# Performance work log

Hardware: AMD Instinct MI355X
Metric: run time of the kernel (lower is better)

## Reference

```python
import jax, jax.numpy as jnp
import numpy as np

Q_LEN, SRC_LEN, B = 512, 2048, 32
Q_SIZE, V_SIZE, OUT_SIZE = 1024, 1024, 1024


def setup_inputs() -> dict:
    key = jax.random.key(0)
    k1, k2, k3, k4, k5, k6 = jax.random.split(key, 6)
    s1 = 1.0 / np.sqrt(Q_SIZE)
    s2 = 1.0 / np.sqrt(Q_SIZE + V_SIZE)
    return {
        "query": jax.random.normal(k1, (Q_LEN, B, Q_SIZE), dtype=jnp.float32),
        "values": jax.random.normal(k2, (SRC_LEN, B, V_SIZE), dtype=jnp.float32),
        "W1": jax.random.uniform(k3, (V_SIZE, Q_SIZE), dtype=jnp.float32, minval=-s1, maxval=s1),
        "b1": jax.random.uniform(k4, (V_SIZE,), dtype=jnp.float32, minval=-s1, maxval=s1),
        "W2": jax.random.uniform(k5, (OUT_SIZE, Q_SIZE + V_SIZE), dtype=jnp.float32, minval=-s2, maxval=s2),
        "b2": jax.random.uniform(k6, (OUT_SIZE,), dtype=jnp.float32, minval=-s2, maxval=s2),
    }


def reference(query, values, W1, b1, W2, b2):
    # query: [q_len, B, Dq]; values: [src_len, B, Dv]
    query_resize = jnp.einsum('qbd,vd->qbv', query, W1) + b1  # [q_len, B, Dv]
    # attn scores: [B, q_len, src_len]
    attn_scores = jnp.einsum('qbv,sbv->bqs', query_resize, values)
    attn = jax.nn.softmax(attn_scores, axis=-1)
    # attended values back to seq-first layout: [q_len, B, Dv]
    attended = jnp.einsum('bqs,sbv->qbv', attn, values)
    query_feed = jnp.concatenate([attended, query], axis=-1)  # [q_len, B, Dv+Dq]
    out = jnp.tanh(jnp.einsum('qbf,of->qbo', query_feed, W2) + b2)
    return out
```

## Files before the change

### kernel.cpp

```cpp
#include <hip/hip_runtime.h>
#include <hip/hip_bf16.h>


typedef __attribute__((ext_vector_type(8))) short bf16x8;
typedef __attribute__((ext_vector_type(4))) float f32x4;

__device__ __forceinline__ ushort f2bf(float x) {
    unsigned u = __builtin_bit_cast(unsigned, x);
    u += 0x7FFFu + ((u >> 16) & 1u);
    return (ushort)(u >> 16);
}
__device__ __forceinline__ float bf2f(ushort h) {
    unsigned u = (unsigned)h << 16;
    return __builtin_bit_cast(float, u);
}
__device__ __forceinline__ void async16(const ushort* g, ushort* l) {
    __builtin_amdgcn_global_load_lds(
        (const __attribute__((address_space(1))) unsigned int*)g,
        (__attribute__((address_space(3))) unsigned int*)l, 16, 0, 0);
}

#define WAITVM(N) asm volatile("s_waitcnt vmcnt(" #N ")" ::: "memory")
#define BAR() do { __builtin_amdgcn_sched_barrier(0); \
                   __builtin_amdgcn_s_barrier();      \
                   __builtin_amdgcn_sched_barrier(0); } while (0)

#define RD_A(QM)                                                              \
  _Pragma("unroll") for (int mi = 0; mi < 4; ++mi)                            \
  _Pragma("unroll") for (int w = 0; w < 2; ++w) {                             \
    const int row_ = (QM)*128 + wmg*64 + mi*16 + lr;                          \
    av[mi][w] = *(const bf16x8*)(bufc + row_*64 + (((w*4+lg)^(lr&7))*8));     \
  }
#define RD_B(QN)                                                              \
  _Pragma("unroll") for (int nj = 0; nj < 2; ++nj)                            \
  _Pragma("unroll") for (int w = 0; w < 2; ++w) {                             \
    const int row_ = (QN)*128 + wnd*32 + nj*16 + lr;                          \
    bv[nj][w] = *(const bf16x8*)(bufc + 16384 + row_*64 + (((w*4+lg)^(lr&7))*8)); \
  }
#define MM(QM,QN)                                                             \
  __builtin_amdgcn_s_setprio(1);                                              \
  _Pragma("unroll") for (int w = 0; w < 2; ++w)                               \
  _Pragma("unroll") for (int mi = 0; mi < 4; ++mi)                            \
  _Pragma("unroll") for (int nj = 0; nj < 2; ++nj)                            \
    acc[(QM)*4+mi][(QN)*2+nj] = __builtin_amdgcn_mfma_f32_16x16x32_bf16(      \
        av[mi][w], bv[nj][w], acc[(QM)*4+mi][(QN)*2+nj], 0, 0, 0);            \
  __builtin_amdgcn_s_setprio(0);

template<int OUTMODE>
__global__ __launch_bounds__(512, 2) void gemm8p(
    const ushort* __restrict__ A0s, const ushort* __restrict__ A1s, const ushort* __restrict__ A2s,
    const ushort* __restrict__ B0s, const ushort* __restrict__ B1s, const ushort* __restrict__ B2s,
    long lda, long ldb, int tps, int nseg,
    const float* __restrict__ bias,
    float* __restrict__ Cf, ushort* __restrict__ Chi, ushort* __restrict__ Clo,
    long ldc, long sAb, long sBb, long sCb)
{
    __shared__ ushort lds[2][32768];

    const int t   = threadIdx.x;
    const int l   = t & 63;
    const int wid = t >> 6;
    const int lr  = l & 15;
    const int lg  = l >> 4;
    const int wmg = wid >> 2;
    const int wnd = wid & 3;

    const int gx = gridDim.x, gy = gridDim.y;
    const int nwg = gx * gy * gridDim.z;
    int w0 = ((int)blockIdx.z * gy + (int)blockIdx.y) * gx + (int)blockIdx.x;
    w0 = (w0 & 7) * (nwg >> 3) + (w0 >> 3);
    const int bx = w0 % gx;
    const int by = (w0 / gx) % gy;
    const int bz = w0 / (gx * gy);

    const long m0 = (long)by * 256;
    const long n0 = (long)bx * 256;

    const ushort* Asg[3] = { A0s + (long)bz * sAb, A1s + (long)bz * sAb, A2s + (long)bz * sAb };
    const ushort* Bsg[3] = { B0s + (long)bz * sBb, B1s + (long)bz * sBb, B2s + (long)bz * sBb };
    const int NTt = nseg * tps;

    const int  rA = t >> 3;
    const long cS = (long)((t & 7) ^ (rA & 7)) * 8;

    auto STAGE = [&](int kt1, bool isB, int half, int destoff) {
        int s2 = (kt1 >= tps) + (kt1 >= 2 * tps);
        long ko = (long)(kt1 - s2 * tps) * 64;
        const ushort* base = isB ? Bsg[s2] : Asg[s2];
        long ld = isB ? ldb : lda;
        long rb = isB ? n0 : m0;
        const ushort* src = base + (rb + half * 128 + rA) * ld + ko + cS;
        ushort* d = &lds[kt1 & 1][destoff + t * 8];
        async16(src, d);
        async16(src + 64 * ld, d + 4096);
    };

    const f32x4 zero = {0.f, 0.f, 0.f, 0.f};
    f32x4 acc[8][4];
#pragma unroll
    for (int i = 0; i < 8; ++i)
#pragma unroll
        for (int j = 0; j < 4; ++j) acc[i][j] = zero;

    STAGE(0, false, 0, 0);
    STAGE(0, true,  0, 16384);
    STAGE(0, true,  1, 24576);
    STAGE(0, false, 1, 8192);

    bf16x8 av[4][2], bv[2][2];

    for (int kt = 0; kt < NTt - 1; ++kt) {
        const ushort* bufc = &lds[kt & 1][0];
        WAITVM(4); BAR();
        STAGE(kt + 1, false, 0, 0);
        RD_A(0); RD_B(0); MM(0, 0);
        WAITVM(4); BAR();
        STAGE(kt + 1, true, 0, 16384);
        RD_B(1); MM(0, 1);
        WAITVM(4); BAR();
        STAGE(kt + 1, true, 1, 24576);
        RD_A(1); MM(1, 1);
        BAR();
        STAGE(kt + 1, false, 1, 8192);
        RD_B(0); MM(1, 0);
    }
    {
        const ushort* bufc = &lds[(NTt - 1) & 1][0];
        WAITVM(4); BAR(); RD_A(0); RD_B(0); MM(0, 0);
        WAITVM(2); BAR(); RD_B(1); MM(0, 1);
        WAITVM(0); BAR(); RD_A(1); MM(1, 1);
        BAR();            RD_B(0); MM(1, 0);
    }

    float*  Cfb = Cf  ? (Cf  + (long)bz * sCb) : nullptr;
    ushort* Chb = Chi ? (Chi + (long)bz * sCb) : nullptr;
    ushort* Clb = Clo ? (Clo + (long)bz * sCb) : nullptr;
#pragma unroll
    for (int qn = 0; qn < 2; ++qn)
#pragma unroll
    for (int nj = 0; nj < 2; ++nj) {
        long n = n0 + qn * 128 + wnd * 32 + nj * 16 + lr;
        float bvs = 0.f;
        if (OUTMODE == 3) bvs = bias[n];
        if (OUTMODE == 2) { if (bias) bvs = bias[n]; }
#pragma unroll
        for (int qm = 0; qm < 2; ++qm)
#pragma unroll
        for (int mi = 0; mi < 4; ++mi) {
            long mb = m0 + qm * 128 + wmg * 64 + mi * 16 + lg * 4;
#pragma unroll
            for (int r = 0; r < 4; ++r) {
                float x = acc[qm * 4 + mi][qn * 2 + nj][r] + bvs;
                long idx = (mb + r) * ldc + n;
                if (OUTMODE == 3) {
                    Cfb[idx] = tanhf(x);
                } else if (OUTMODE == 2) {
                    ushort h = f2bf(x);
                    Chb[idx] = h;
                    if (Clb) Clb[idx] = f2bf(x - bf2f(h));
                } else {
                    Cfb[idx] = x;
                }
            }
        }
    }
}

__global__ __launch_bounds__(256) void split_pair_k(
    const float* __restrict__ in, ushort* __restrict__ hi, ushort* __restrict__ lo, long n4)
{
    long i = (long)blockIdx.x * 256 + threadIdx.x;
    const long stride = (long)gridDim.x * 256;
    for (; i < n4; i += stride) {
        float4 x = ((const float4*)in)[i];
        ushort4 h, lw;
        h.x = f2bf(x.x); lw.x = f2bf(x.x - bf2f(h.x));
        h.y = f2bf(x.y); lw.y = f2bf(x.y - bf2f(h.y));
        h.z = f2bf(x.z); lw.z = f2bf(x.z - bf2f(h.z));
        h.w = f2bf(x.w); lw.w = f2bf(x.w - bf2f(h.w));
        ((ushort4*)hi)[i] = h;
        ((ushort4*)lo)[i] = lw;
    }
}

__global__ __launch_bounds__(256) void values_conv_k(
    const float* __restrict__ values,
    ushort* __restrict__ vhi, ushort* __restrict__ vlo, ushort* __restrict__ vT,
    int b0, int gc)
{
    __shared__ float tile[64][65];
    const int t  = threadIdx.x;
    const int s0 = blockIdx.x * 64;
    const int v0 = blockIdx.y * 64;
    const int bi = blockIdx.z;
    const int b  = b0 + bi;
#pragma unroll
    for (int i = 0; i < 4; ++i) {
        int c = t + i * 256;
        int r = c >> 4;
        int qq = c & 15;
        float4 x = *(const float4*)(values + ((long)(s0 + r) * 32 + b) * 1024 + v0 + qq * 4);
        ushort4 h, lw;
        h.x = f2bf(x.x); lw.x = f2bf(x.x - bf2f(h.x));
        h.y = f2bf(x.y); lw.y = f2bf(x.y - bf2f(h.y));
        h.z = f2bf(x.z); lw.z = f2bf(x.z - bf2f(h.z));
        h.w = f2bf(x.w); lw.w = f2bf(x.w - bf2f(h.w));
        long rowoff = ((long)(s0 + r) * gc + bi) * 1024 + v0 + qq * 4;
        *(ushort4*)(vhi + rowoff) = h;
        *(ushort4*)(vlo + rowoff) = lw;
        tile[r][qq * 4 + 0] = x.x;
        tile[r][qq * 4 + 1] = x.y;
        tile[r][qq * 4 + 2] = x.z;
        tile[r][qq * 4 + 3] = x.w;
    }
    __syncthreads();
    const int vr = t >> 2;
    const int ss = (t & 3) * 16;
    ushort* dst = vT + ((long)bi * 1024 + v0 + vr) * 2048 + s0 + ss;
#pragma unroll
    for (int j = 0; j < 4; ++j) {
        ushort4 o;
        o.x = f2bf(tile[ss + j * 4 + 0][vr]);
        o.y = f2bf(tile[ss + j * 4 + 1][vr]);
        o.z = f2bf(tile[ss + j * 4 + 2][vr]);
        o.w = f2bf(tile[ss + j * 4 + 3][vr]);
        *(ushort4*)(dst + j * 4) = o;
    }
}

__global__ __launch_bounds__(256) void softmax2048b_k(
    const float* __restrict__ S, ushort* __restrict__ P)
{
    __shared__ float red[4];
    const long row = blockIdx.x;
    const float* p = S + row * 2048 + threadIdx.x * 8;
    float4 a = ((const float4*)p)[0];
    float4 b = ((const float4*)p)[1];

    float m = fmaxf(fmaxf(fmaxf(a.x, a.y), fmaxf(a.z, a.w)),
                    fmaxf(fmaxf(b.x, b.y), fmaxf(b.z, b.w)));
#pragma unroll
    for (int off = 32; off; off >>= 1) m = fmaxf(m, __shfl_xor(m, off));
    int wid = threadIdx.x >> 6;
    if ((threadIdx.x & 63) == 0) red[wid] = m;
    __syncthreads();
    m = fmaxf(fmaxf(red[0], red[1]), fmaxf(red[2], red[3]));
    __syncthreads();

    a.x = __expf(a.x - m); a.y = __expf(a.y - m);
    a.z = __expf(a.z - m); a.w = __expf(a.w - m);
    b.x = __expf(b.x - m); b.y = __expf(b.y - m);
    b.z = __expf(b.z - m); b.w = __expf(b.w - m);

    float s = a.x + a.y + a.z + a.w + b.x + b.y + b.z + b.w;
#pragma unroll
    for (int off = 32; off; off >>= 1) s += __shfl_xor(s, off);
    if ((threadIdx.x & 63) == 0) red[wid] = s;
    __syncthreads();
    s = red[0] + red[1] + red[2] + red[3];
    float inv = 1.0f / s;

    ushort* qp = P + row * 2048 + threadIdx.x * 8;
    ushort4 oA, oB;
    oA.x = f2bf(a.x * inv); oA.y = f2bf(a.y * inv);
    oA.z = f2bf(a.z * inv); oA.w = f2bf(a.w * inv);
    oB.x = f2bf(b.x * inv); oB.y = f2bf(b.y * inv);
    oB.z = f2bf(b.z * inv); oB.w = f2bf(b.w * inv);
    ((ushort4*)qp)[0] = oA;
    ((ushort4*)qp)[1] = oB;
}

#define BMF 128
#define BNF 128
#define BKF 16

template<bool NT, int MODE>
__global__ __launch_bounds__(256) void gemm_f32(
    const float* __restrict__ A, const float* __restrict__ A2, int Ksplit,
    const float* __restrict__ Bm, const float* __restrict__ bias,
    float* __restrict__ C,
    long lda, long ldb, long ldc, int K,
    long sAb, long sBb, long sCb)
{
    __shared__ float As[BKF][BMF + 4];
    __shared__ float Bs[BKF][BNF + 4];

    const int bz = blockIdx.z;
    const float* Ab  = A + (long)bz * sAb;
    const float* A2b = A2 ? (A2 + (long)bz * sAb) : nullptr;
    const float* Bb  = Bm + (long)bz * sBb;
    float*       Cb  = C + (long)bz * sCb;

    const int m0 = blockIdx.y * BMF;
    const int n0 = blockIdx.x * BNF;
    const int t  = threadIdx.x;
    const int tx = t & 15;
    const int ty = t >> 4;

    float acc[8][8];
#pragma unroll
    for (int i = 0; i < 8; ++i)
#pragma unroll
        for (int j = 0; j < 8; ++j) acc[i][j] = 0.f;

    for (int k0 = 0; k0 < K; k0 += BKF) {
        const float* Asrc = (A2b && k0 >= Ksplit) ? (A2b - Ksplit) : Ab;
#pragma unroll
        for (int c = 0; c < 2; ++c) {
            int chunk = t + c * 256;
            int row = chunk >> 2;
            int kq  = chunk & 3;
            float4 v = *(const float4*)(Asrc + (long)(m0 + row) * lda + k0 + kq * 4);
            As[kq * 4 + 0][row] = v.x;
            As[kq * 4 + 1][row] = v.y;
            As[kq * 4 + 2][row] = v.z;
            As[kq * 4 + 3][row] = v.w;
        }
        if (NT) {
#pragma unroll
            for (int c = 0; c < 2; ++c) {
                int chunk = t + c * 256;
                int row = chunk >> 2;
                int kq  = chunk & 3;
                float4 v = *(const float4*)(Bb + (long)(n0 + row) * ldb + k0 + kq * 4);
                Bs[kq * 4 + 0][row] = v.x;
                Bs[kq * 4 + 1][row] = v.y;
                Bs[kq * 4 + 2][row] = v.z;
                Bs[kq * 4 + 3][row] = v.w;
            }
        } else {
#pragma unroll
            for (int c = 0; c < 2; ++c) {
                int chunk = t + c * 256;
                int kr = chunk >> 5;
                int vq = chunk & 31;
                float4 v = *(const float4*)(Bb + (long)(k0 + kr) * ldb + n0 + vq * 4);
                *(float4*)&Bs[kr][vq * 4] = v;
            }
        }
        __syncthreads();

#pragma unroll
        for (int k = 0; k < BKF; ++k) {
            float4 a0 = *(const float4*)&As[k][ty * 8];
            float4 a1 = *(const float4*)&As[k][ty * 8 + 4];
            float4 b0 = *(const float4*)&Bs[k][tx * 8];
            float4 b1 = *(const float4*)&Bs[k][tx * 8 + 4];
            float ar[8] = {a0.x, a0.y, a0.z, a0.w, a1.x, a1.y, a1.z, a1.w};
            float br[8] = {b0.x, b0.y, b0.z, b0.w, b1.x, b1.y, b1.z, b1.w};
#pragma unroll
            for (int i = 0; i < 8; ++i)
#pragma unroll
                for (int j = 0; j < 8; ++j)
                    acc[i][j] += ar[i] * br[j];
        }
        __syncthreads();
    }

    float brow[8];
    if (MODE >= 1) {
#pragma unroll
        for (int j = 0; j < 8; ++j) brow[j] = bias[n0 + tx * 8 + j];
    }
#pragma unroll
    for (int i = 0; i < 8; ++i) {
        long row = m0 + ty * 8 + i;
        float v[8];
#pragma unroll
        for (int j = 0; j < 8; ++j) {
            float x = acc[i][j];
            if (MODE >= 1) x += brow[j];
            if (MODE == 2) x = tanhf(x);
            v[j] = x;
        }
        float4* dst = (float4*)&Cb[row * ldc + n0 + tx * 8];
        dst[0] = make_float4(v[0], v[1], v[2], v[3]);
        dst[1] = make_float4(v[4], v[5], v[6], v[7]);
    }
}

__global__ __launch_bounds__(256) void softmax2048(float* __restrict__ S)
{
    __shared__ float red[4];
    float* p = S + (long)blockIdx.x * 2048 + threadIdx.x * 8;
    float4 a = ((float4*)p)[0];
    float4 b = ((float4*)p)[1];

    float m = fmaxf(fmaxf(fmaxf(a.x, a.y), fmaxf(a.z, a.w)),
                    fmaxf(fmaxf(b.x, b.y), fmaxf(b.z, b.w)));
#pragma unroll
    for (int off = 32; off; off >>= 1) m = fmaxf(m, __shfl_xor(m, off));
    int wid = threadIdx.x >> 6;
    if ((threadIdx.x & 63) == 0) red[wid] = m;
    __syncthreads();
    m = fmaxf(fmaxf(red[0], red[1]), fmaxf(red[2], red[3]));
    __syncthreads();

    a.x = __expf(a.x - m); a.y = __expf(a.y - m);
    a.z = __expf(a.z - m); a.w = __expf(a.w - m);
    b.x = __expf(b.x - m); b.y = __expf(b.y - m);
    b.z = __expf(b.z - m); b.w = __expf(b.w - m);

    float s = a.x + a.y + a.z + a.w + b.x + b.y + b.z + b.w;
#pragma unroll
    for (int off = 32; off; off >>= 1) s += __shfl_xor(s, off);
    if ((threadIdx.x & 63) == 0) red[wid] = s;
    __syncthreads();
    s = red[0] + red[1] + red[2] + red[3];
    float inv = 1.0f / s;

    a.x *= inv; a.y *= inv; a.z *= inv; a.w *= inv;
    b.x *= inv; b.y *= inv; b.z *= inv; b.w *= inv;
    ((float4*)p)[0] = a;
    ((float4*)p)[1] = b;
}

extern "C" void kernel_launch(void* const* d_in, const int* in_sizes, int n_in,
                              void* d_out, int out_size, void* d_ws, size_t ws_size,
                              hipStream_t stream)
{
    const float* query  = (const float*)d_in[0];
    const float* values = (const float*)d_in[1];
    const float* W1     = (const float*)d_in[2];
    const float* b1     = (const float*)d_in[3];
    const float* W2     = (const float*)d_in[4];
    const float* b2     = (const float*)d_in[5];
    float* out = (float*)d_out;

    const int Bc = 32, QL = 512, SL = 2048, D = 1024, F = 2048;
    const long R = (long)QL * Bc;

    char* p = (char*)d_ws;
    auto take = [&](size_t bytes) -> char* {
        char* r = p;
        p += (bytes + 255) & ~(size_t)255;
        return r;
    };

    ushort* q_hi  = (ushort*)take((size_t)R * D * 2);
    ushort* q_lo  = (ushort*)take((size_t)R * D * 2);
    ushort* w1_hi = (ushort*)take((size_t)D * D * 2);
    ushort* w1_lo = (ushort*)take((size_t)D * D * 2);
    ushort* w2_hi = (ushort*)take((size_t)D * F * 2);
    ushort* w2_lo = (ushort*)take((size_t)D * F * 2);
    ushort* qr_hi = (ushort*)take((size_t)R * D * 2);
    ushort* qr_lo = (ushort*)take((size_t)R * D * 2);
    ushort* at_hi = (ushort*)take((size_t)R * D * 2);
    size_t fixedBytes = (size_t)(p - (char*)d_ws);

    const size_t perBatch = (size_t)SL * D * 2 * 3 + (size_t)QL * SL * 4 + (size_t)QL * SL * 2 + 2048;
    long availB = (long)ws_size - (long)fixedBytes;
    int g = availB > 0 ? (int)(availB / (long)perBatch) : 0;
    if (g > 32) g = 32;

    if (g >= 1) {
        ushort* vals_hi = (ushort*)take((size_t)SL * D * 2 * g);
        ushort* vals_lo = (ushort*)take((size_t)SL * D * 2 * g);
        ushort* vT      = (ushort*)take((size_t)SL * D * 2 * g);
        float*  scores  = (float*) take((size_t)QL * SL * 4 * g);
        ushort* P       = (ushort*)take((size_t)QL * SL * 2 * g);

        split_pair_k<<<2048, 256, 0, stream>>>(query, q_hi, q_lo, R * D / 4);
        split_pair_k<<<1024, 256, 0, stream>>>(W1, w1_hi, w1_lo, (long)D * D / 4);
        split_pair_k<<<1024, 256, 0, stream>>>(W2, w2_hi, w2_lo, (long)D * F / 4);

        gemm8p<2><<<dim3(D / 256, R / 256, 1), 512, 0, stream>>>(
            q_hi, q_hi, q_lo, w1_hi, w1_lo, w1_hi,
            D, D, 16, 3, b1,
            nullptr, qr_hi, qr_lo,
            D, 0, 0, 0);

        for (int b0 = 0; b0 < Bc; b0 += g) {
            int gc = (Bc - b0 < g) ? (Bc - b0) : g;

            values_conv_k<<<dim3(SL / 64, D / 64, gc), 256, 0, stream>>>(
                values, vals_hi, vals_lo, vT, b0, gc);

            gemm8p<0><<<dim3(SL / 256, QL / 256, gc), 512, 0, stream>>>(
                qr_hi + (size_t)b0 * D, qr_hi + (size_t)b0 * D, qr_lo + (size_t)b0 * D,
                vals_hi, vals_lo, vals_hi,
                (long)Bc * D, (long)gc * D, 16, 3, nullptr,
                scores, nullptr, nullptr,
                SL, D, D, (long)QL * SL);

            softmax2048b_k<<<gc * QL, 256, 0, stream>>>(scores, P);

            gemm8p<2><<<dim3(D / 256, QL / 256, gc), 512, 0, stream>>>(
                P, P, P, vT, vT, vT,
                SL, SL, 32, 1, nullptr,
                nullptr, at_hi + (size_t)b0 * D, nullptr,
                (long)Bc * D, (long)QL * SL, (long)D * SL, D);
        }

        gemm8p<3><<<dim3(D / 256, R / 256, 1), 512, 0, stream>>>(
            at_hi, q_hi, q_hi, w2_hi, w2_hi + 1024, w2_hi,
            D, F, 16, 2, b2,
            out, nullptr, nullptr,
            D, 0, 0, 0);
        return;
    }

    float* qr = (float*)d_ws;
    size_t qrBytes = (size_t)R * D * sizeof(float);
    float* sc = (float*)((char*)d_ws + qrBytes);
    size_t scPerB = (size_t)QL * SL * sizeof(float);

    int grp = 32;
    if (ws_size < qrBytes + 32 * scPerB) {
        size_t avail = ws_size > qrBytes ? ws_size - qrBytes : 0;
        grp = (int)(avail / scPerB);
        if (grp < 1)  grp = 1;
        if (grp > 32) grp = 32;
    }

    {
        dim3 gd(D / BNF, R / BMF, 1);
        gemm_f32<true, 1><<<gd, 256, 0, stream>>>(
            query, nullptr, 1 << 30, W1, b1, qr,
            D, D, D, D, 0, 0, 0);
    }
    for (int b0 = 0; b0 < Bc; b0 += grp) {
        int gg = (Bc - b0 < grp) ? (Bc - b0) : grp;
        {
            dim3 gd(SL / BNF, QL / BMF, gg);
            gemm_f32<true, 0><<<gd, 256, 0, stream>>>(
                qr + (size_t)b0 * D, nullptr, 1 << 30,
                values + (size_t)b0 * D, nullptr, sc,
                (long)Bc * D, (long)Bc * D, SL, D,
                D, D, (long)QL * SL);
        }
        softmax2048<<<gg * QL, 256, 0, stream>>>(sc);
        {
            dim3 gd(D / BNF, QL / BMF, gg);
            gemm_f32<false, 0><<<gd, 256, 0, stream>>>(
                sc, nullptr, 1 << 30,
                values + (size_t)b0 * D, nullptr, qr + (size_t)b0 * D,
                SL, (long)Bc * D, (long)Bc * D, SL,
                (long)QL * SL, D, D);
        }
    }
    {
        dim3 gd(D / BNF, R / BMF, 1);
        gemm_f32<true, 2><<<gd, 256, 0, stream>>>(
            qr, query, D, W2, b2, out,
            D, 2048, D, 2048, 0, 0, 0);
    }
}
```

Before: 641.4 us.

## Issue LDS fragment reads before async stage and barrier-sync ahead of MFMA

Restructures the 8-phase GEMM main loop so LDS fragment reads for each quadrant are issued before the next global-to-LDS async stage and a barrier, then waits on lgkmcnt before the MFMA block. B fragments for quadrant 0 are kept in a separate register set (bv0) so the final MM(1,0) reuses them instead of re-reading LDS. The aim is to overlap LDS reads with global loads and remove one redundant LDS read per iteration. In exchange it adds an extra barrier per phase and more register pressure under the 2-blocks-per-CU launch bound.

```diff
diff --git a/kernel.cpp b/kernel.cpp
--- a/kernel.cpp
+++ b/kernel.cpp
@@ -21,9 +21,12 @@
 }
 
 #define WAITVM(N) asm volatile("s_waitcnt vmcnt(" #N ")" ::: "memory")
-#define BAR() do { __builtin_amdgcn_sched_barrier(0); \
-                   __builtin_amdgcn_s_barrier();      \
-                   __builtin_amdgcn_sched_barrier(0); } while (0)
+#define SBAR()    __builtin_amdgcn_sched_barrier(0)
+#define ENDBAR()  do { SBAR(); __builtin_amdgcn_s_barrier(); SBAR(); } while (0)
+#define PREMM()   do { SBAR(); __builtin_amdgcn_s_barrier();                  \
+                       asm volatile("s_waitcnt lgkmcnt(0)" ::: "memory");     \
+                       SBAR(); __builtin_amdgcn_s_setprio(1); } while (0)
+#define POSTMM()  __builtin_amdgcn_s_setprio(0)
 
 #define RD_A(QM)                                                              \
   _Pragma("unroll") for (int mi = 0; mi < 4; ++mi)                            \
@@ -31,20 +34,18 @@
     const int row_ = (QM)*128 + wmg*64 + mi*16 + lr;                          \
     av[mi][w] = *(const bf16x8*)(bufc + row_*64 + (((w*4+lg)^(lr&7))*8));     \
   }
-#define RD_B(QN)                                                              \
+#define RD_B(QN, DST)                                                         \
   _Pragma("unroll") for (int nj = 0; nj < 2; ++nj)                            \
   _Pragma("unroll") for (int w = 0; w < 2; ++w) {                             \
     const int row_ = (QN)*128 + wnd*32 + nj*16 + lr;                          \
-    bv[nj][w] = *(const bf16x8*)(bufc + 16384 + row_*64 + (((w*4+lg)^(lr&7))*8)); \
+    DST[nj][w] = *(const bf16x8*)(bufc + 16384 + row_*64 + (((w*4+lg)^(lr&7))*8)); \
   }
-#define MM(QM,QN)                                                             \
-  __builtin_amdgcn_s_setprio(1);                                              \
+#define MM(QM, QN, BSRC)                                                      \
   _Pragma("unroll") for (int w = 0; w < 2; ++w)                               \
   _Pragma("unroll") for (int mi = 0; mi < 4; ++mi)                            \
   _Pragma("unroll") for (int nj = 0; nj < 2; ++nj)                            \
     acc[(QM)*4+mi][(QN)*2+nj] = __builtin_amdgcn_mfma_f32_16x16x32_bf16(      \
-        av[mi][w], bv[nj][w], acc[(QM)*4+mi][(QN)*2+nj], 0, 0, 0);            \
-  __builtin_amdgcn_s_setprio(0);
+        av[mi][w], BSRC[nj][w], acc[(QM)*4+mi][(QN)*2+nj], 0, 0, 0);
 
 template<int OUTMODE>
 __global__ __launch_bounds__(512, 2) void gemm8p(
@@ -106,30 +107,41 @@
     STAGE(0, true,  0, 16384);
     STAGE(0, true,  1, 24576);
     STAGE(0, false, 1, 8192);
-
-    bf16x8 av[4][2], bv[2][2];
+    WAITVM(4);
+    ENDBAR();
+
+    bf16x8 av[4][2], bv[2][2], bv0[2][2];
 
     for (int kt = 0; kt < NTt - 1; ++kt) {
         const ushort* bufc = &lds[kt & 1][0];
-        WAITVM(4); BAR();
+        RD_A(0); RD_B(0, bv0);
         STAGE(kt + 1, false, 0, 0);
-        RD_A(0); RD_B(0); MM(0, 0);
-        WAITVM(4); BAR();
+        PREMM(); MM(0, 0, bv0); POSTMM();
+        WAITVM(4); ENDBAR();
+        RD_B(1, bv);
         STAGE(kt + 1, true, 0, 16384);
-        RD_B(1); MM(0, 1);
-        WAITVM(4); BAR();
+        PREMM(); MM(0, 1, bv); POSTMM();
+        WAITVM(4); ENDBAR();
+        RD_A(1);
         STAGE(kt + 1, true, 1, 24576);
-        RD_A(1); MM(1, 1);
-        BAR();
+        PREMM(); MM(1, 1, bv); POSTMM();
+        ENDBAR();
         STAGE(kt + 1, false, 1, 8192);
-        RD_B(0); MM(1, 0);
+        PREMM(); MM(1, 0, bv0); POSTMM();
+        WAITVM(4); ENDBAR();
     }
     {
         const ushort* bufc = &lds[(NTt - 1) & 1][0];
-        WAITVM(4); BAR(); RD_A(0); RD_B(0); MM(0, 0);
-        WAITVM(2); BAR(); RD_B(1); MM(0, 1);
-        WAITVM(0); BAR(); RD_A(1); MM(1, 1);
-        BAR();            RD_B(0); MM(1, 0);
+        RD_A(0); RD_B(0, bv0);
+        PREMM(); MM(0, 0, bv0); POSTMM();
+        WAITVM(2); ENDBAR();
+        RD_B(1, bv);
+        PREMM(); MM(0, 1, bv); POSTMM();
+        WAITVM(0); ENDBAR();
+        RD_A(1);
+        PREMM(); MM(1, 1, bv); POSTMM();
+        ENDBAR();
+        PREMM(); MM(1, 0, bv0); POSTMM();
     }
 
     float*  Cfb = Cf  ? (Cf  + (long)bz * sCb) : nullptr;
```

Measured after the change: 641.1 us. About the same (-0.1%).

## Restructure GEMM main loop into two phases and fuse split kernels

Applied to the files above, without the earlier changes.

The bf16 GEMM inner loop goes from four barrier-separated quarter-phases to two. Each phase issues two staging loads and reads both B quarter-tiles into separate register sets, so each A read feeds two MFMA blocks and there are fewer barriers and LDS reloads per k-step. The three fp32-to-bf16 hi/lo split launches become a single kernel that walks all three arrays, saving launch overhead. The cost is extra register pressure from the second B fragment set and changed vmcnt waits that must still match the async load ordering.

```diff
diff --git a/kernel.cpp b/kernel.cpp
--- a/kernel.cpp
+++ b/kernel.cpp
@@ -21,9 +21,10 @@
 }
 
 #define WAITVM(N) asm volatile("s_waitcnt vmcnt(" #N ")" ::: "memory")
-#define BAR() do { __builtin_amdgcn_sched_barrier(0); \
-                   __builtin_amdgcn_s_barrier();      \
-                   __builtin_amdgcn_sched_barrier(0); } while (0)
+#define BARF() do { __builtin_amdgcn_sched_barrier(0);          \
+                    __builtin_amdgcn_s_barrier();               \
+                    __builtin_amdgcn_sched_barrier(0);          \
+                    asm volatile("" ::: "memory"); } while (0)
 
 #define RD_A(QM)                                                              \
   _Pragma("unroll") for (int mi = 0; mi < 4; ++mi)                            \
@@ -31,20 +32,18 @@
     const int row_ = (QM)*128 + wmg*64 + mi*16 + lr;                          \
     av[mi][w] = *(const bf16x8*)(bufc + row_*64 + (((w*4+lg)^(lr&7))*8));     \
   }
-#define RD_B(QN)                                                              \
+#define RD_B(QN, DST)                                                         \
   _Pragma("unroll") for (int nj = 0; nj < 2; ++nj)                            \
   _Pragma("unroll") for (int w = 0; w < 2; ++w) {                             \
     const int row_ = (QN)*128 + wnd*32 + nj*16 + lr;                          \
-    bv[nj][w] = *(const bf16x8*)(bufc + 16384 + row_*64 + (((w*4+lg)^(lr&7))*8)); \
+    DST[nj][w] = *(const bf16x8*)(bufc + 16384 + row_*64 + (((w*4+lg)^(lr&7))*8)); \
   }
-#define MM(QM,QN)                                                             \
-  __builtin_amdgcn_s_setprio(1);                                              \
+#define MM(QM, QN, BSRC)                                                      \
   _Pragma("unroll") for (int w = 0; w < 2; ++w)                               \
   _Pragma("unroll") for (int mi = 0; mi < 4; ++mi)                            \
   _Pragma("unroll") for (int nj = 0; nj < 2; ++nj)                            \
     acc[(QM)*4+mi][(QN)*2+nj] = __builtin_amdgcn_mfma_f32_16x16x32_bf16(      \
-        av[mi][w], bv[nj][w], acc[(QM)*4+mi][(QN)*2+nj], 0, 0, 0);            \
-  __builtin_amdgcn_s_setprio(0);
+        av[mi][w], BSRC[nj][w], acc[(QM)*4+mi][(QN)*2+nj], 0, 0, 0);
 
 template<int OUTMODE>
 __global__ __launch_bounds__(512, 2) void gemm8p(
@@ -107,29 +106,37 @@
     STAGE(0, true,  1, 24576);
     STAGE(0, false, 1, 8192);
 
-    bf16x8 av[4][2], bv[2][2];
+    bf16x8 av[4][2], bv0[2][2], bv1[2][2];
 
     for (int kt = 0; kt < NTt - 1; ++kt) {
         const ushort* bufc = &lds[kt & 1][0];
-        WAITVM(4); BAR();
+        WAITVM(2); BARF();
         STAGE(kt + 1, false, 0, 0);
-        RD_A(0); RD_B(0); MM(0, 0);
-        WAITVM(4); BAR();
-        STAGE(kt + 1, true, 0, 16384);
-        RD_B(1); MM(0, 1);
-        WAITVM(4); BAR();
-        STAGE(kt + 1, true, 1, 24576);
-        RD_A(1); MM(1, 1);
-        BAR();
+        STAGE(kt + 1, true,  0, 16384);
+        RD_A(0); RD_B(0, bv0); RD_B(1, bv1);
+        __builtin_amdgcn_s_setprio(1);
+        MM(0, 0, bv0); MM(0, 1, bv1);
+        __builtin_amdgcn_s_setprio(0);
+        WAITVM(4); BARF();
+        STAGE(kt + 1, true,  1, 24576);
         STAGE(kt + 1, false, 1, 8192);
-        RD_B(0); MM(1, 0);
+        RD_A(1);
+        __builtin_amdgcn_s_setprio(1);
+        MM(1, 0, bv0); MM(1, 1, bv1);
+        __builtin_amdgcn_s_setprio(0);
     }
     {
         const ushort* bufc = &lds[(NTt - 1) & 1][0];
-        WAITVM(4); BAR(); RD_A(0); RD_B(0); MM(0, 0);
-        WAITVM(2); BAR(); RD_B(1); MM(0, 1);
-        WAITVM(0); BAR(); RD_A(1); MM(1, 1);
-        BAR();            RD_B(0); MM(1, 0);
+        WAITVM(2); BARF();
+        RD_A(0); RD_B(0, bv0); RD_B(1, bv1);
+        __builtin_amdgcn_s_setprio(1);
+        MM(0, 0, bv0); MM(0, 1, bv1);
+        __builtin_amdgcn_s_setprio(0);
+        WAITVM(0); BARF();
+        RD_A(1);
+        __builtin_amdgcn_s_setprio(1);
+        MM(1, 0, bv0); MM(1, 1, bv1);
+        __builtin_amdgcn_s_setprio(0);
     }
 
     float*  Cfb = Cf  ? (Cf  + (long)bz * sCb) : nullptr;
@@ -166,20 +173,27 @@
     }
 }
 
-__global__ __launch_bounds__(256) void split_pair_k(
-    const float* __restrict__ in, ushort* __restrict__ hi, ushort* __restrict__ lo, long n4)
+__global__ __launch_bounds__(256) void split3_k(
+    const float* __restrict__ a0, ushort* __restrict__ h0, ushort* __restrict__ l0, long n0,
+    const float* __restrict__ a1, ushort* __restrict__ h1, ushort* __restrict__ l1, long n1,
+    const float* __restrict__ a2, ushort* __restrict__ h2, ushort* __restrict__ l2, long n2)
 {
     long i = (long)blockIdx.x * 256 + threadIdx.x;
     const long stride = (long)gridDim.x * 256;
-    for (; i < n4; i += stride) {
-        float4 x = ((const float4*)in)[i];
+    const long tot = n0 + n1 + n2;
+    for (; i < tot; i += stride) {
+        const float* src; ushort* hh; ushort* ll; long j = i;
+        if (j < n0)           { src = a0; hh = h0; ll = l0; }
+        else if (j < n0 + n1) { j -= n0; src = a1; hh = h1; ll = l1; }
+        else                  { j -= n0 + n1; src = a2; hh = h2; ll = l2; }
+        float4 x = ((const float4*)src)[j];
         ushort4 h, lw;
         h.x = f2bf(x.x); lw.x = f2bf(x.x - bf2f(h.x));
         h.y = f2bf(x.y); lw.y = f2bf(x.y - bf2f(h.y));
         h.z = f2bf(x.z); lw.z = f2bf(x.z - bf2f(h.z));
         h.w = f2bf(x.w); lw.w = f2bf(x.w - bf2f(h.w));
-        ((ushort4*)hi)[i] = h;
-        ((ushort4*)lo)[i] = lw;
+        ((ushort4*)hh)[j] = h;
+        ((ushort4*)ll)[j] = lw;
     }
 }
 
@@ -460,9 +474,10 @@
         float*  scores  = (float*) take((size_t)QL * SL * 4 * g);
         ushort* P       = (ushort*)take((size_t)QL * SL * 2 * g);
 
-        split_pair_k<<<2048, 256, 0, stream>>>(query, q_hi, q_lo, R * D / 4);
-        split_pair_k<<<1024, 256, 0, stream>>>(W1, w1_hi, w1_lo, (long)D * D / 4);
-        split_pair_k<<<1024, 256, 0, stream>>>(W2, w2_hi, w2_lo, (long)D * F / 4);
+        split3_k<<<2048, 256, 0, stream>>>(
+            query, q_hi, q_lo, R * D / 4,
+            W1, w1_hi, w1_lo, (long)D * D / 4,
+            W2, w2_hi, w2_lo, (long)D * F / 4);
 
         gemm8p<2><<<dim3(D / 256, R / 256, 1), 512, 0, stream>>>(
             q_hi, q_hi, q_lo, w1_hi, w1_lo, w1_hi,
```

New measurement: 646.6 us. Within noise of the previous version (+0.8%).
